# Kernel optimization log

Measured on AMD Instinct MI355X. Metric: run time of the kernel, lower is better.

Reference implementation:

```python
import jax, jax.numpy as jnp
import numpy as np

NEG_INF = -1e8  # masked_fill value from the torch code
EPS_DICE = 0.001
EPS_DIV = 1e-5
LOSS_FACTOR = 1.0  # loss['factor']


def conv2d(x, w, b, pad):
    # x: [B,C,H,W], w: [O,I,kh,kw] (OIHW), b: [O]
    y = jax.lax.conv_general_dilated(
        x, w, window_strides=(1, 1), padding=[(pad, pad), (pad, pad)],
        dimension_numbers=("NCHW", "OIHW", "NCHW"))
    return y + b[None, :, None, None]


def setup_inputs() -> dict:
    key = jax.random.key(0)
    ks = jax.random.split(key, 12)
    B, C, H, W = 2, 256, 64, 64
    s = 0.05  # small init scale to keep logits in a sane range
    inp = {
        "feats": jax.random.normal(ks[0], (B, C, H, W), jnp.float32),
        "masks": jax.random.randint(ks[1], (B, H, W), 0, 2).astype(jnp.float32),
        "layouts": jax.random.randint(ks[2], (B, H, W), 0, 16).astype(jnp.int32),
        "w_pre0": jax.random.normal(ks[3], (C, C, 3, 3), jnp.float32) * s,
        "b_pre0": jax.random.normal(ks[4], (C,), jnp.float32) * s,
        "w_pre1": jax.random.normal(ks[5], (C, C, 3, 3), jnp.float32) * s,
        "b_pre1": jax.random.normal(ks[6], (C,), jnp.float32) * s,
        "w_kernel": jax.random.normal(ks[7], (C + 1, C, 1, 1), jnp.float32) * s,
        "b_kernel": jax.random.normal(ks[8], (C + 1,), jnp.float32) * s,
        "w_feats": jax.random.normal(ks[9], (C, C, 1, 1), jnp.float32) * s,
        "b_feats": jax.random.normal(ks[10], (C,), jnp.float32) * s,
    }
    return inp


def reference(feats, masks, layouts, w_pre0, b_pre0, w_pre1, b_pre1,
              w_kernel, b_kernel, w_feats, b_feats):
    B, C, H, W = feats.shape
    # pre_kernel_convs: two 3x3 conv + ReLU
    h = jax.nn.relu(conv2d(feats, w_pre0, b_pre0, pad=1))
    h = jax.nn.relu(conv2d(h, w_pre1, b_pre1, pad=1))
    kernels = conv2d(h, w_kernel, b_kernel, pad=0)          # [B, C+1, H, W]
    f = conv2d(feats, w_feats, b_feats, pad=0)               # [B, C,   H, W]
    # permute(0,2,3,1).reshape(B, H*W, C+1): per-cell dynamic 1x1 conv params
    kernels = kernels.transpose(0, 2, 3, 1).reshape(B, H * W, C + 1)
    kw = kernels[..., :C]                                    # [B, P, C]
    kb = kernels[..., C]                                     # [B, P]
    # grouped 1x1 conv == batched matmul over channel dim
    logits = jnp.einsum("bpc,bchw->bphw", kw, f) + kb[:, :, None, None]
    logits = jnp.where(masks[:, None, :, :] > 0, logits, NEG_INF)  # [B,P,H,W]

    # --- training loss (dice, div='all') ---
    # segm_labels[b, r*W+c] = (layouts[b] == layouts[b,r,c])
    flat = layouts.reshape(B, H * W)
    labels = (layouts[:, None, :, :] == flat[:, :, None, None]).astype(logits.dtype)
    p = jax.nn.sigmoid(logits)
    d = 2.0 * (p * labels) / (p * p + EPS_DICE + labels * labels + EPS_DICE)
    loss_el = 1.0 - d                                        # [B, P, H, W]
    m_flat = masks.reshape(B, H * W)
    num = ((loss_el * masks[:, None, :, :]).sum((-1, -2)) * m_flat).sum(-1)  # [B]
    grid = masks.sum((1, 2))
    loss = (LOSS_FACTOR * num / (grid * grid + EPS_DIV)).mean()
    return logits, loss
```

## Files before the change

### kernel.cpp

```cpp
#include <hip/hip_runtime.h>
#include <hip/hip_bf16.h>
#include <math.h>

typedef __attribute__((ext_vector_type(8))) short bf16x8;
typedef __attribute__((ext_vector_type(4))) float f32x4;
typedef __hip_bfloat16 bf16_t;

#define NEG_INF_V -100000000.0f

__device__ __forceinline__ void gload16(const void* g, void* l) {
  __builtin_amdgcn_global_load_lds(
      (const __attribute__((address_space(1))) unsigned int*)g,
      (__attribute__((address_space(3))) unsigned int*)l, 16, 0, 0);
}

__global__ __launch_bounds__(256) void pad_cast_k(
    const float* __restrict__ feats, bf16_t* __restrict__ x_pad) {
  __shared__ float s[64][65];
  const int t = threadIdx.x;
  const int y = blockIdx.x, c0 = blockIdx.y * 64, b = blockIdx.z;
  const float* fb = feats + ((size_t)b * 256 + c0) * 4096 + y * 64;
  for (int i = t; i < 64 * 64; i += 256) {
    int ci = i >> 6, x = i & 63;
    s[ci][x] = fb[(size_t)ci * 4096 + x];
  }
  __syncthreads();
  bf16_t* xp = x_pad + (size_t)b * (66 * 66 * 256) + ((size_t)(y + 1) * 66 + 1) * 256 + c0;
  for (int i = t; i < 64 * 64; i += 256) {
    int x = i >> 6, ci = i & 63;
    xp[(size_t)x * 256 + ci] = __float2bfloat16(s[ci][x]);
  }
}

__global__ __launch_bounds__(256) void castw3_k(
    const float* __restrict__ w0, const float* __restrict__ w1,
    bf16_t* __restrict__ o0, bf16_t* __restrict__ o1) {
  const int co = blockIdx.x, t = threadIdx.x;
  const float* ws = blockIdx.y ? w1 : w0;
  bf16_t* wd = blockIdx.y ? o1 : o0;
#pragma unroll
  for (int k = 0; k < 9; ++k)
    wd[(size_t)co * 2304 + k * 256 + t] = __float2bfloat16(ws[((size_t)co * 256 + t) * 9 + k]);
}

__global__ __launch_bounds__(256) void castw1_k(
    const float* __restrict__ wk, const float* __restrict__ wf,
    bf16_t* __restrict__ ok, bf16_t* __restrict__ of) {
  int i = blockIdx.x * 256 + threadIdx.x;
  if (i < 257 * 256) ok[i] = __float2bfloat16(wk[i]);
  else { int j = i - 257 * 256; if (j < 256 * 256) of[j] = __float2bfloat16(wf[j]); }
}

__global__ __launch_bounds__(256) void conv3x3_mfma_k(
    const bf16_t* __restrict__ xpad, const bf16_t* __restrict__ wr,
    const float* __restrict__ bias, bf16_t* __restrict__ out,
    int out_row_stride, int out_base, long out_bstride) {
  __shared__ __align__(16) short ldsA[64 * 32];
  __shared__ __align__(16) short ldsB[128 * 32];
  const int t = threadIdx.x, w = t >> 6, lane = t & 63;
  const int y = blockIdx.x, co0 = blockIdx.y * 128, b = blockIdx.z;
  const bf16_t* xb = xpad + (size_t)b * (66 * 66 * 256);
  const int wm = w >> 1, wn = w & 1;
  f32x4 acc[2][4] = {};
  const int spix = w * 16 + (lane >> 2);
  const int scio = (lane & 3) * 8;
  const int sbco = w * 32 + (lane >> 2);
  const int aoff = (wm * 32 + (lane & 15)) * 32 + (lane >> 4) * 8;
  const int boff = (wn * 64 + (lane & 15)) * 32 + (lane >> 4) * 8;
  short* ldsAw = &ldsA[w * 512];
  short* ldsBw0 = &ldsB[(w * 32) * 32];
  short* ldsBw1 = &ldsB[(w * 32 + 16) * 32];

  for (int ks = 0; ks < 72; ++ks) {
    const int kpos = ks >> 3, cik = (ks & 7) * 32;
    const int ky = (kpos * 11) >> 5, kx = kpos - 3 * ky;
    gload16(xb + ((size_t)(y + ky) * 66 + spix + kx) * 256 + cik + scio, ldsAw);
    const bf16_t* gb = wr + (size_t)(co0 + sbco) * 2304 + kpos * 256 + cik + scio;
    gload16(gb, ldsBw0);
    gload16(gb + 16 * 2304, ldsBw1);
    __syncthreads();
    bf16x8 af0 = *(const bf16x8*)&ldsA[aoff];
    bf16x8 af1 = *(const bf16x8*)&ldsA[aoff + 512];
#pragma unroll
    for (int n = 0; n < 4; ++n) {
      bf16x8 bf = *(const bf16x8*)&ldsB[boff + n * 512];
      acc[0][n] = __builtin_amdgcn_mfma_f32_16x16x32_bf16(af0, bf, acc[0][n], 0, 0, 0);
      acc[1][n] = __builtin_amdgcn_mfma_f32_16x16x32_bf16(af1, bf, acc[1][n], 0, 0, 0);
    }
    __syncthreads();
  }
  bf16_t* ob = out + (size_t)b * out_bstride;
  float bv[4];
#pragma unroll
  for (int n = 0; n < 4; ++n) bv[n] = bias[co0 + wn * 64 + n * 16 + (lane & 15)];
#pragma unroll
  for (int m = 0; m < 2; ++m) {
#pragma unroll
    for (int r = 0; r < 4; ++r) {
      int x = wm * 32 + m * 16 + (lane >> 4) * 4 + r;
      size_t ra = (size_t)out_base + (size_t)y * out_row_stride + (size_t)x * 256 + co0 + wn * 64 + (lane & 15);
#pragma unroll
      for (int n = 0; n < 4; ++n) {
        float v = acc[m][n][r] + bv[n];
        ob[ra + n * 16] = __float2bfloat16(fmaxf(v, 0.f));
      }
    }
  }
}

template <bool KER>
__global__ __launch_bounds__(256) void conv1x1_mfma_k(
    const bf16_t* __restrict__ in, const bf16_t* __restrict__ wt,
    const float* __restrict__ bias, bf16_t* __restrict__ outw,
    float* __restrict__ outkb, int A0, int AS, long in_bstride, int comax) {
  __shared__ __align__(16) short ldsA[64 * 32];
  __shared__ __align__(16) short ldsB[128 * 32];
  const int t = threadIdx.x, w = t >> 6, lane = t & 63;
  const int y = blockIdx.x, co0 = blockIdx.y * 128, b = blockIdx.z;
  const bf16_t* inb = in + (size_t)b * in_bstride;
  const int wm = w >> 1, wn = w & 1;
  f32x4 acc[2][4] = {};
  const int spix = w * 16 + (lane >> 2);
  const int scio = (lane & 3) * 8;
  const int sbco = co0 + w * 32 + (lane >> 2);
  const int aoff = (wm * 32 + (lane & 15)) * 32 + (lane >> 4) * 8;
  const int boff = (wn * 64 + (lane & 15)) * 32 + (lane >> 4) * 8;
  short* ldsAw = &ldsA[w * 512];
  short* ldsBw0 = &ldsB[(w * 32) * 32];
  short* ldsBw1 = &ldsB[(w * 32 + 16) * 32];

  for (int ks = 0; ks < 8; ++ks) {
    const int cik = ks * 32;
    gload16(inb + (size_t)A0 + (size_t)y * AS + (size_t)spix * 256 + cik + scio, ldsAw);
    int c0r = min(sbco, comax - 1), c1r = min(sbco + 16, comax - 1);
    gload16(wt + (size_t)c0r * 256 + cik + scio, ldsBw0);
    gload16(wt + (size_t)c1r * 256 + cik + scio, ldsBw1);
    __syncthreads();
    bf16x8 af0 = *(const bf16x8*)&ldsA[aoff];
    bf16x8 af1 = *(const bf16x8*)&ldsA[aoff + 512];
#pragma unroll
    for (int n = 0; n < 4; ++n) {
      bf16x8 bf = *(const bf16x8*)&ldsB[boff + n * 512];
      acc[0][n] = __builtin_amdgcn_mfma_f32_16x16x32_bf16(af0, bf, acc[0][n], 0, 0, 0);
      acc[1][n] = __builtin_amdgcn_mfma_f32_16x16x32_bf16(af1, bf, acc[1][n], 0, 0, 0);
    }
    __syncthreads();
  }
#pragma unroll
  for (int m = 0; m < 2; ++m) {
#pragma unroll
    for (int r = 0; r < 4; ++r) {
      int x = wm * 32 + m * 16 + (lane >> 4) * 4 + r;
      int prow = y * 64 + x;
#pragma unroll
      for (int n = 0; n < 4; ++n) {
        int co = co0 + wn * 64 + n * 16 + (lane & 15);
        float v = acc[m][n][r] + bias[min(co, comax - 1)];
        if (KER) {
          if (co < 256) outw[((size_t)b * 4096 + prow) * 256 + co] = __float2bfloat16(v);
          else if (co == 256) outkb[(size_t)b * 4096 + prow] = v;
        } else {
          outw[((size_t)b * 4096 + prow) * 256 + co] = __float2bfloat16(v);
        }
      }
    }
  }
}

__global__ __launch_bounds__(256) void logits_mfma_k(
    const bf16_t* __restrict__ kwt, const float* __restrict__ kb,
    const bf16_t* __restrict__ fft, const float* __restrict__ masks,
    const int* __restrict__ layouts, float* __restrict__ out,
    float* __restrict__ partial) {
  __shared__ __align__(16) short ldsA[64 * 32];
  __shared__ __align__(16) short ldsB[128 * 32];
  const int t = threadIdx.x, w = t >> 6, lane = t & 63;
  const int p0 = blockIdx.x * 64, q0 = blockIdx.y * 128, b = blockIdx.z;
  const bf16_t* ab = kwt + (size_t)b * (4096 * 256);
  const bf16_t* bb = fft + (size_t)b * (4096 * 256);
  const int wm = w >> 1, wn = w & 1;
  f32x4 acc[2][4] = {};
  const int spix = w * 16 + (lane >> 2);
  const int scio = (lane & 3) * 8;
  const int sbq = w * 32 + (lane >> 2);
  const int aoff = (wm * 32 + (lane & 15)) * 32 + (lane >> 4) * 8;
  const int boff = (wn * 64 + (lane & 15)) * 32 + (lane >> 4) * 8;
  short* ldsAw = &ldsA[w * 512];
  short* ldsBw0 = &ldsB[(w * 32) * 32];
  short* ldsBw1 = &ldsB[(w * 32 + 16) * 32];

  for (int ks = 0; ks < 8; ++ks) {
    const int cik = ks * 32;
    gload16(ab + (size_t)(p0 + spix) * 256 + cik + scio, ldsAw);
    gload16(bb + (size_t)(q0 + sbq) * 256 + cik + scio, ldsBw0);
    gload16(bb + (size_t)(q0 + sbq + 16) * 256 + cik + scio, ldsBw1);
    __syncthreads();
    bf16x8 af0 = *(const bf16x8*)&ldsA[aoff];
    bf16x8 af1 = *(const bf16x8*)&ldsA[aoff + 512];
#pragma unroll
    for (int n = 0; n < 4; ++n) {
      bf16x8 bf = *(const bf16x8*)&ldsB[boff + n * 512];
      acc[0][n] = __builtin_amdgcn_mfma_f32_16x16x32_bf16(af0, bf, acc[0][n], 0, 0, 0);
      acc[1][n] = __builtin_amdgcn_mfma_f32_16x16x32_bf16(af1, bf, acc[1][n], 0, 0, 0);
    }
    __syncthreads();
  }

  float mq[4];
  int layq[4];
#pragma unroll
  for (int n = 0; n < 4; ++n) {
    int q = q0 + wn * 64 + n * 16 + (lane & 15);
    mq[n] = masks[b * 4096 + q];
    layq[n] = layouts[b * 4096 + q];
  }
  float sl[8];
#pragma unroll
  for (int i = 0; i < 8; ++i) sl[i] = 0.f;
  float* outb = out + (size_t)b * 4096 * 4096;
#pragma unroll
  for (int m = 0; m < 2; ++m) {
#pragma unroll
    for (int r = 0; r < 4; ++r) {
      int p = p0 + wm * 32 + m * 16 + (lane >> 4) * 4 + r;
      float kbv = kb[b * 4096 + p];
      int layp = layouts[b * 4096 + p];
      float s = 0.f;
      size_t ra = (size_t)p * 4096 + q0 + wn * 64 + (lane & 15);
#pragma unroll
      for (int n = 0; n < 4; ++n) {
        float lg = (mq[n] > 0.f) ? (acc[m][n][r] + kbv) : NEG_INF_V;
        outb[ra + n * 16] = lg;
        float pz = 1.f / (1.f + __expf(-lg));
        float lab = (layp == layq[n]) ? 1.f : 0.f;
        float d = 2.f * pz * lab / (pz * pz + lab + 0.002f);
        s += (1.f - d) * mq[n];
      }
      sl[m * 4 + r] = s;
    }
  }
#pragma unroll
  for (int i = 0; i < 8; ++i) {
    float v = sl[i];
    v += __shfl_xor(v, 1); v += __shfl_xor(v, 2);
    v += __shfl_xor(v, 4); v += __shfl_xor(v, 8);
    sl[i] = v;
  }
  if ((lane & 15) == 0) {
    int qt = blockIdx.y * 2 + wn;
#pragma unroll
    for (int m = 0; m < 2; ++m)
#pragma unroll
      for (int r = 0; r < 4; ++r) {
        int p = p0 + wm * 32 + m * 16 + (lane >> 4) * 4 + r;
        partial[((size_t)b * 4096 + p) * 64 + qt] = sl[m * 4 + r];
      }
  }
}

__global__ __launch_bounds__(256) void rowsum_k(
    const float* __restrict__ partial, const float* __restrict__ masks,
    float* __restrict__ accum) {
  const int t = threadIdx.x, w = t >> 6, lane = t & 63;
  const int idx = blockIdx.x * 256 + t;
  const int b = idx >> 12;
  const float* pp = partial + (size_t)idx * 64;
  float s = 0.f;
#pragma unroll
  for (int k = 0; k < 64; ++k) s += pp[k];
  float mp = masks[idx];
  float num = s * mp;
#pragma unroll
  for (int off = 32; off; off >>= 1) {
    num += __shfl_down(num, off);
    mp += __shfl_down(mp, off);
  }
  __shared__ float sn[4], sm[4];
  if (lane == 0) { sn[w] = num; sm[w] = mp; }
  __syncthreads();
  if (t == 0) {
    atomicAdd(&accum[b * 2], sn[0] + sn[1] + sn[2] + sn[3]);
    atomicAdd(&accum[b * 2 + 1], sm[0] + sm[1] + sm[2] + sm[3]);
  }
}

__global__ void loss_final_k(const float* __restrict__ accum, float* __restrict__ out_loss) {
  if (threadIdx.x == 0) {
    float l0 = accum[0] / (accum[1] * accum[1] + 1e-5f);
    float l1 = accum[2] / (accum[3] * accum[3] + 1e-5f);
    out_loss[0] = 0.5f * (l0 + l1);
  }
}

extern "C" void kernel_launch(void* const* d_in, const int* in_sizes, int n_in,
                              void* d_out, int out_size, void* d_ws, size_t ws_size,
                              hipStream_t stream) {
  const float* feats = (const float*)d_in[0];
  const float* masks = (const float*)d_in[1];
  const int* layouts = (const int*)d_in[2];
  const float* w_pre0 = (const float*)d_in[3];
  const float* b_pre0 = (const float*)d_in[4];
  const float* w_pre1 = (const float*)d_in[5];
  const float* b_pre1 = (const float*)d_in[6];
  const float* w_kernel = (const float*)d_in[7];
  const float* b_kernel = (const float*)d_in[8];
  const float* w_feats = (const float*)d_in[9];
  const float* b_feats = (const float*)d_in[10];

  bf16_t* x_pad = (bf16_t*)d_ws;
  bf16_t* h1p = x_pad + 2 * 1115136;
  bf16_t* h2 = h1p + 2 * 1115136;
  bf16_t* w0r = h2 + 2 * 1048576;
  bf16_t* w1r = w0r + 589824;
  bf16_t* wkb = w1r + 589824;
  bf16_t* wfb = wkb + 65792;
  bf16_t* kwt = wfb + 65536;
  bf16_t* fft = kwt + 2 * 1048576;
  float* kb = (float*)(fft + 2 * 1048576);
  float* partial = kb + 8192;
  float* accum = partial + 524288;
  float* out = (float*)d_out;

  hipMemsetAsync(x_pad, 0, (size_t)4 * 1115136 * sizeof(bf16_t), stream);
  hipMemsetAsync(accum, 0, 4 * sizeof(float), stream);

  pad_cast_k<<<dim3(64, 4, 2), 256, 0, stream>>>(feats, x_pad);
  castw3_k<<<dim3(256, 2), 256, 0, stream>>>(w_pre0, w_pre1, w0r, w1r);
  castw1_k<<<dim3(514), 256, 0, stream>>>(w_kernel, w_feats, wkb, wfb);

  conv3x3_mfma_k<<<dim3(64, 2, 2), 256, 0, stream>>>(
      x_pad, w0r, b_pre0, h1p, 66 * 256, 67 * 256, 1115136L);
  conv3x3_mfma_k<<<dim3(64, 2, 2), 256, 0, stream>>>(
      h1p, w1r, b_pre1, h2, 64 * 256, 0, 1048576L);

  conv1x1_mfma_k<true><<<dim3(64, 3, 2), 256, 0, stream>>>(
      h2, wkb, b_kernel, kwt, kb, 0, 16384, 1048576L, 257);
  conv1x1_mfma_k<false><<<dim3(64, 2, 2), 256, 0, stream>>>(
      x_pad, wfb, b_feats, fft, nullptr, 67 * 256, 66 * 256, 1115136L, 256);

  logits_mfma_k<<<dim3(64, 32, 2), 256, 0, stream>>>(
      kwt, kb, fft, masks, layouts, out, partial);

  rowsum_k<<<dim3(32), 256, 0, stream>>>(partial, masks, accum);
  loss_final_k<<<1, 64, 0, stream>>>(accum, out + (size_t)2 * 4096 * 4096);
}
```

Measured before the change: 304.0 us.

## Double-buffer LDS with XOR swizzle and K=64 stages in MFMA GEMM kernels

Rewrites the conv3x3, conv1x1 and logits MFMA kernels so that they load K-slices of 64 into double-buffered LDS. The next slice is prefetched while the current one is computed, which halves the barriers per K step. LDS reads use an XOR swizzle to avoid bank conflicts. The conv kernels also shrink the output-channel tile from 128 to 64 and double the grid, giving more blocks for occupancy in exchange for more re-reads of the activations.

```diff
diff --git a/kernel.cpp b/kernel.cpp
--- a/kernel.cpp
+++ b/kernel.cpp
@@ -12,6 +12,10 @@
   __builtin_amdgcn_global_load_lds(
       (const __attribute__((address_space(1))) unsigned int*)g,
       (__attribute__((address_space(3))) unsigned int*)l, 16, 0, 0);
+}
+
+__device__ __forceinline__ bf16x8 swzread(const short* base, int r, int c) {
+  return *(const bf16x8*)(base + ((r * 8 + (c ^ (r & 7))) << 3));
 }
 
 __global__ __launch_bounds__(256) void pad_cast_k(
@@ -55,57 +59,75 @@
     const bf16_t* __restrict__ xpad, const bf16_t* __restrict__ wr,
     const float* __restrict__ bias, bf16_t* __restrict__ out,
     int out_row_stride, int out_base, long out_bstride) {
-  __shared__ __align__(16) short ldsA[64 * 32];
-  __shared__ __align__(16) short ldsB[128 * 32];
+  __shared__ __align__(16) short ldsA[2][4096];
+  __shared__ __align__(16) short ldsB[2][4096];
   const int t = threadIdx.x, w = t >> 6, lane = t & 63;
-  const int y = blockIdx.x, co0 = blockIdx.y * 128, b = blockIdx.z;
+  const int y = blockIdx.x, co0 = blockIdx.y * 64, b = blockIdx.z;
   const bf16_t* xb = xpad + (size_t)b * (66 * 66 * 256);
   const int wm = w >> 1, wn = w & 1;
-  f32x4 acc[2][4] = {};
-  const int spix = w * 16 + (lane >> 2);
-  const int scio = (lane & 3) * 8;
-  const int sbco = w * 32 + (lane >> 2);
-  const int aoff = (wm * 32 + (lane & 15)) * 32 + (lane >> 4) * 8;
-  const int boff = (wn * 64 + (lane & 15)) * 32 + (lane >> 4) * 8;
-  short* ldsAw = &ldsA[w * 512];
-  short* ldsBw0 = &ldsB[(w * 32) * 32];
-  short* ldsBw1 = &ldsB[(w * 32 + 16) * 32];
-
-  for (int ks = 0; ks < 72; ++ks) {
-    const int kpos = ks >> 3, cik = (ks & 7) * 32;
-    const int ky = (kpos * 11) >> 5, kx = kpos - 3 * ky;
-    gload16(xb + ((size_t)(y + ky) * 66 + spix + kx) * 256 + cik + scio, ldsAw);
-    const bf16_t* gb = wr + (size_t)(co0 + sbco) * 2304 + kpos * 256 + cik + scio;
-    gload16(gb, ldsBw0);
-    gload16(gb + 16 * 2304, ldsBw1);
+  f32x4 acc[2][2] = {};
+
+  int ar[2], ac[2];
+#pragma unroll
+  for (int p = 0; p < 2; ++p) {
+    int u = (p * 4 + w) * 64 + lane;
+    ar[p] = u >> 3;
+    ac[p] = ((u & 7) ^ ((u >> 3) & 7)) * 8;
+  }
+  const int fr = lane & 15, fc = lane >> 4;
+
+  auto stage = [&](int ks, int buf) {
+    int kpos = ks >> 2, cik = (ks & 3) * 64;
+    int ky = (kpos * 11) >> 5, kx = kpos - 3 * ky;
+#pragma unroll
+    for (int p = 0; p < 2; ++p) {
+      gload16(xb + ((size_t)(y + ky) * 66 + (ar[p] + kx)) * 256 + cik + ac[p],
+              &ldsA[buf][(p * 4 + w) * 512]);
+      gload16(wr + (size_t)(co0 + ar[p]) * 2304 + kpos * 256 + cik + ac[p],
+              &ldsB[buf][(p * 4 + w) * 512]);
+    }
+  };
+  auto compute = [&](int buf) {
+#pragma unroll
+    for (int kk = 0; kk < 2; ++kk) {
+      bf16x8 af[2], bfr[2];
+#pragma unroll
+      for (int m = 0; m < 2; ++m) af[m] = swzread(ldsA[buf], wm * 32 + m * 16 + fr, kk * 4 + fc);
+#pragma unroll
+      for (int n = 0; n < 2; ++n) bfr[n] = swzread(ldsB[buf], wn * 32 + n * 16 + fr, kk * 4 + fc);
+#pragma unroll
+      for (int m = 0; m < 2; ++m)
+#pragma unroll
+        for (int n = 0; n < 2; ++n)
+          acc[m][n] = __builtin_amdgcn_mfma_f32_16x16x32_bf16(af[m], bfr[n], acc[m][n], 0, 0, 0);
+    }
+  };
+
+  stage(0, 0);
+  __syncthreads();
+  for (int ks = 0; ks < 35; ++ks) {
+    stage(ks + 1, (ks + 1) & 1);
+    compute(ks & 1);
     __syncthreads();
-    bf16x8 af0 = *(const bf16x8*)&ldsA[aoff];
-    bf16x8 af1 = *(const bf16x8*)&ldsA[aoff + 512];
-#pragma unroll
-    for (int n = 0; n < 4; ++n) {
-      bf16x8 bf = *(const bf16x8*)&ldsB[boff + n * 512];
-      acc[0][n] = __builtin_amdgcn_mfma_f32_16x16x32_bf16(af0, bf, acc[0][n], 0, 0, 0);
-      acc[1][n] = __builtin_amdgcn_mfma_f32_16x16x32_bf16(af1, bf, acc[1][n], 0, 0, 0);
-    }
-    __syncthreads();
-  }
+  }
+  compute(1);
+
   bf16_t* ob = out + (size_t)b * out_bstride;
-  float bv[4];
-#pragma unroll
-  for (int n = 0; n < 4; ++n) bv[n] = bias[co0 + wn * 64 + n * 16 + (lane & 15)];
-#pragma unroll
-  for (int m = 0; m < 2; ++m) {
+  float bv[2];
+#pragma unroll
+  for (int n = 0; n < 2; ++n) bv[n] = bias[co0 + wn * 32 + n * 16 + fr];
+#pragma unroll
+  for (int m = 0; m < 2; ++m)
 #pragma unroll
     for (int r = 0; r < 4; ++r) {
-      int x = wm * 32 + m * 16 + (lane >> 4) * 4 + r;
-      size_t ra = (size_t)out_base + (size_t)y * out_row_stride + (size_t)x * 256 + co0 + wn * 64 + (lane & 15);
-#pragma unroll
-      for (int n = 0; n < 4; ++n) {
+      int x = wm * 32 + m * 16 + fc * 4 + r;
+      size_t ra = (size_t)out_base + (size_t)y * out_row_stride + (size_t)x * 256 + co0 + wn * 32 + fr;
+#pragma unroll
+      for (int n = 0; n < 2; ++n) {
         float v = acc[m][n][r] + bv[n];
         ob[ra + n * 16] = __float2bfloat16(fmaxf(v, 0.f));
       }
     }
-  }
 }
 
 template <bool KER>
@@ -113,48 +135,67 @@
     const bf16_t* __restrict__ in, const bf16_t* __restrict__ wt,
     const float* __restrict__ bias, bf16_t* __restrict__ outw,
     float* __restrict__ outkb, int A0, int AS, long in_bstride, int comax) {
-  __shared__ __align__(16) short ldsA[64 * 32];
-  __shared__ __align__(16) short ldsB[128 * 32];
+  __shared__ __align__(16) short ldsA[2][4096];
+  __shared__ __align__(16) short ldsB[2][4096];
   const int t = threadIdx.x, w = t >> 6, lane = t & 63;
-  const int y = blockIdx.x, co0 = blockIdx.y * 128, b = blockIdx.z;
+  const int y = blockIdx.x, co0 = blockIdx.y * 64, b = blockIdx.z;
   const bf16_t* inb = in + (size_t)b * in_bstride;
   const int wm = w >> 1, wn = w & 1;
-  f32x4 acc[2][4] = {};
-  const int spix = w * 16 + (lane >> 2);
-  const int scio = (lane & 3) * 8;
-  const int sbco = co0 + w * 32 + (lane >> 2);
-  const int aoff = (wm * 32 + (lane & 15)) * 32 + (lane >> 4) * 8;
-  const int boff = (wn * 64 + (lane & 15)) * 32 + (lane >> 4) * 8;
-  short* ldsAw = &ldsA[w * 512];
-  short* ldsBw0 = &ldsB[(w * 32) * 32];
-  short* ldsBw1 = &ldsB[(w * 32 + 16) * 32];
-
-  for (int ks = 0; ks < 8; ++ks) {
-    const int cik = ks * 32;
-    gload16(inb + (size_t)A0 + (size_t)y * AS + (size_t)spix * 256 + cik + scio, ldsAw);
-    int c0r = min(sbco, comax - 1), c1r = min(sbco + 16, comax - 1);
-    gload16(wt + (size_t)c0r * 256 + cik + scio, ldsBw0);
-    gload16(wt + (size_t)c1r * 256 + cik + scio, ldsBw1);
+  f32x4 acc[2][2] = {};
+
+  int ar[2], ac[2];
+#pragma unroll
+  for (int p = 0; p < 2; ++p) {
+    int u = (p * 4 + w) * 64 + lane;
+    ar[p] = u >> 3;
+    ac[p] = ((u & 7) ^ ((u >> 3) & 7)) * 8;
+  }
+  const int fr = lane & 15, fc = lane >> 4;
+
+  auto stage = [&](int ks, int buf) {
+    int cik = ks * 64;
+#pragma unroll
+    for (int p = 0; p < 2; ++p) {
+      gload16(inb + (size_t)A0 + (size_t)y * AS + (size_t)ar[p] * 256 + cik + ac[p],
+              &ldsA[buf][(p * 4 + w) * 512]);
+      gload16(wt + (size_t)min(co0 + ar[p], comax - 1) * 256 + cik + ac[p],
+              &ldsB[buf][(p * 4 + w) * 512]);
+    }
+  };
+  auto compute = [&](int buf) {
+#pragma unroll
+    for (int kk = 0; kk < 2; ++kk) {
+      bf16x8 af[2], bfr[2];
+#pragma unroll
+      for (int m = 0; m < 2; ++m) af[m] = swzread(ldsA[buf], wm * 32 + m * 16 + fr, kk * 4 + fc);
+#pragma unroll
+      for (int n = 0; n < 2; ++n) bfr[n] = swzread(ldsB[buf], wn * 32 + n * 16 + fr, kk * 4 + fc);
+#pragma unroll
+      for (int m = 0; m < 2; ++m)
+#pragma unroll
+        for (int n = 0; n < 2; ++n)
+          acc[m][n] = __builtin_amdgcn_mfma_f32_16x16x32_bf16(af[m], bfr[n], acc[m][n], 0, 0, 0);
+    }
+  };
+
+  stage(0, 0);
+  __syncthreads();
+  for (int ks = 0; ks < 3; ++ks) {
+    stage(ks + 1, (ks + 1) & 1);
+    compute(ks & 1);
     __syncthreads();
-    bf16x8 af0 = *(const bf16x8*)&ldsA[aoff];
-    bf16x8 af1 = *(const bf16x8*)&ldsA[aoff + 512];
-#pragma unroll
-    for (int n = 0; n < 4; ++n) {
-      bf16x8 bf = *(const bf16x8*)&ldsB[boff + n * 512];
-      acc[0][n] = __builtin_amdgcn_mfma_f32_16x16x32_bf16(af0, bf, acc[0][n], 0, 0, 0);
-      acc[1][n] = __builtin_amdgcn_mfma_f32_16x16x32_bf16(af1, bf, acc[1][n], 0, 0, 0);
-    }
-    __syncthreads();
-  }
-#pragma unroll
-  for (int m = 0; m < 2; ++m) {
+  }
+  compute(1);
+
+#pragma unroll
+  for (int m = 0; m < 2; ++m)
 #pragma unroll
     for (int r = 0; r < 4; ++r) {
-      int x = wm * 32 + m * 16 + (lane >> 4) * 4 + r;
+      int x = wm * 32 + m * 16 + fc * 4 + r;
       int prow = y * 64 + x;
 #pragma unroll
-      for (int n = 0; n < 4; ++n) {
-        int co = co0 + wn * 64 + n * 16 + (lane & 15);
+      for (int n = 0; n < 2; ++n) {
+        int co = co0 + wn * 32 + n * 16 + fr;
         float v = acc[m][n][r] + bias[min(co, comax - 1)];
         if (KER) {
           if (co < 256) outw[((size_t)b * 4096 + prow) * 256 + co] = __float2bfloat16(v);
@@ -164,7 +205,6 @@
         }
       }
     }
-  }
 }
 
 __global__ __launch_bounds__(256) void logits_mfma_k(
@@ -172,45 +212,69 @@
     const bf16_t* __restrict__ fft, const float* __restrict__ masks,
     const int* __restrict__ layouts, float* __restrict__ out,
     float* __restrict__ partial) {
-  __shared__ __align__(16) short ldsA[64 * 32];
-  __shared__ __align__(16) short ldsB[128 * 32];
+  __shared__ __align__(16) short ldsA[2][4096];
+  __shared__ __align__(16) short ldsB[2][8192];
   const int t = threadIdx.x, w = t >> 6, lane = t & 63;
   const int p0 = blockIdx.x * 64, q0 = blockIdx.y * 128, b = blockIdx.z;
   const bf16_t* ab = kwt + (size_t)b * (4096 * 256);
   const bf16_t* bb = fft + (size_t)b * (4096 * 256);
   const int wm = w >> 1, wn = w & 1;
   f32x4 acc[2][4] = {};
-  const int spix = w * 16 + (lane >> 2);
-  const int scio = (lane & 3) * 8;
-  const int sbq = w * 32 + (lane >> 2);
-  const int aoff = (wm * 32 + (lane & 15)) * 32 + (lane >> 4) * 8;
-  const int boff = (wn * 64 + (lane & 15)) * 32 + (lane >> 4) * 8;
-  short* ldsAw = &ldsA[w * 512];
-  short* ldsBw0 = &ldsB[(w * 32) * 32];
-  short* ldsBw1 = &ldsB[(w * 32 + 16) * 32];
-
-  for (int ks = 0; ks < 8; ++ks) {
-    const int cik = ks * 32;
-    gload16(ab + (size_t)(p0 + spix) * 256 + cik + scio, ldsAw);
-    gload16(bb + (size_t)(q0 + sbq) * 256 + cik + scio, ldsBw0);
-    gload16(bb + (size_t)(q0 + sbq + 16) * 256 + cik + scio, ldsBw1);
+
+  int ar[2], ac[2], br[4], bc[4];
+#pragma unroll
+  for (int p = 0; p < 2; ++p) {
+    int u = (p * 4 + w) * 64 + lane;
+    ar[p] = u >> 3;
+    ac[p] = ((u & 7) ^ ((u >> 3) & 7)) * 8;
+  }
+#pragma unroll
+  for (int p = 0; p < 4; ++p) {
+    int u = (p * 4 + w) * 64 + lane;
+    br[p] = u >> 3;
+    bc[p] = ((u & 7) ^ ((u >> 3) & 7)) * 8;
+  }
+  const int fr = lane & 15, fc = lane >> 4;
+
+  auto stage = [&](int ks, int buf) {
+    int cik = ks * 64;
+#pragma unroll
+    for (int p = 0; p < 2; ++p)
+      gload16(ab + (size_t)(p0 + ar[p]) * 256 + cik + ac[p], &ldsA[buf][(p * 4 + w) * 512]);
+#pragma unroll
+    for (int p = 0; p < 4; ++p)
+      gload16(bb + (size_t)(q0 + br[p]) * 256 + cik + bc[p], &ldsB[buf][(p * 4 + w) * 512]);
+  };
+  auto compute = [&](int buf) {
+#pragma unroll
+    for (int kk = 0; kk < 2; ++kk) {
+      bf16x8 af[2], bfr[4];
+#pragma unroll
+      for (int m = 0; m < 2; ++m) af[m] = swzread(ldsA[buf], wm * 32 + m * 16 + fr, kk * 4 + fc);
+#pragma unroll
+      for (int n = 0; n < 4; ++n) bfr[n] = swzread(ldsB[buf], wn * 64 + n * 16 + fr, kk * 4 + fc);
+#pragma unroll
+      for (int m = 0; m < 2; ++m)
+#pragma unroll
+        for (int n = 0; n < 4; ++n)
+          acc[m][n] = __builtin_amdgcn_mfma_f32_16x16x32_bf16(af[m], bfr[n], acc[m][n], 0, 0, 0);
+    }
+  };
+
+  stage(0, 0);
+  __syncthreads();
+  for (int ks = 0; ks < 3; ++ks) {
+    stage(ks + 1, (ks + 1) & 1);
+    compute(ks & 1);
     __syncthreads();
-    bf16x8 af0 = *(const bf16x8*)&ldsA[aoff];
-    bf16x8 af1 = *(const bf16x8*)&ldsA[aoff + 512];
-#pragma unroll
-    for (int n = 0; n < 4; ++n) {
-      bf16x8 bf = *(const bf16x8*)&ldsB[boff + n * 512];
-      acc[0][n] = __builtin_amdgcn_mfma_f32_16x16x32_bf16(af0, bf, acc[0][n], 0, 0, 0);
-      acc[1][n] = __builtin_amdgcn_mfma_f32_16x16x32_bf16(af1, bf, acc[1][n], 0, 0, 0);
-    }
-    __syncthreads();
-  }
+  }
+  compute(1);
 
   float mq[4];
   int layq[4];
 #pragma unroll
   for (int n = 0; n < 4; ++n) {
-    int q = q0 + wn * 64 + n * 16 + (lane & 15);
+    int q = q0 + wn * 64 + n * 16 + fr;
     mq[n] = masks[b * 4096 + q];
     layq[n] = layouts[b * 4096 + q];
   }
@@ -222,11 +286,11 @@
   for (int m = 0; m < 2; ++m) {
 #pragma unroll
     for (int r = 0; r < 4; ++r) {
-      int p = p0 + wm * 32 + m * 16 + (lane >> 4) * 4 + r;
+      int p = p0 + wm * 32 + m * 16 + fc * 4 + r;
       float kbv = kb[b * 4096 + p];
       int layp = layouts[b * 4096 + p];
       float s = 0.f;
-      size_t ra = (size_t)p * 4096 + q0 + wn * 64 + (lane & 15);
+      size_t ra = (size_t)p * 4096 + q0 + wn * 64 + fr;
 #pragma unroll
       for (int n = 0; n < 4; ++n) {
         float lg = (mq[n] > 0.f) ? (acc[m][n][r] + kbv) : NEG_INF_V;
@@ -246,13 +310,13 @@
     v += __shfl_xor(v, 4); v += __shfl_xor(v, 8);
     sl[i] = v;
   }
-  if ((lane & 15) == 0) {
+  if (fr == 0) {
     int qt = blockIdx.y * 2 + wn;
 #pragma unroll
     for (int m = 0; m < 2; ++m)
 #pragma unroll
       for (int r = 0; r < 4; ++r) {
-        int p = p0 + wm * 32 + m * 16 + (lane >> 4) * 4 + r;
+        int p = p0 + wm * 32 + m * 16 + fc * 4 + r;
         partial[((size_t)b * 4096 + p) * 64 + qt] = sl[m * 4 + r];
       }
   }
@@ -328,14 +392,14 @@
   castw3_k<<<dim3(256, 2), 256, 0, stream>>>(w_pre0, w_pre1, w0r, w1r);
   castw1_k<<<dim3(514), 256, 0, stream>>>(w_kernel, w_feats, wkb, wfb);
 
-  conv3x3_mfma_k<<<dim3(64, 2, 2), 256, 0, stream>>>(
+  conv3x3_mfma_k<<<dim3(64, 4, 2), 256, 0, stream>>>(
       x_pad, w0r, b_pre0, h1p, 66 * 256, 67 * 256, 1115136L);
-  conv3x3_mfma_k<<<dim3(64, 2, 2), 256, 0, stream>>>(
+  conv3x3_mfma_k<<<dim3(64, 4, 2), 256, 0, stream>>>(
       h1p, w1r, b_pre1, h2, 64 * 256, 0, 1048576L);
 
-  conv1x1_mfma_k<true><<<dim3(64, 3, 2), 256, 0, stream>>>(
+  conv1x1_mfma_k<true><<<dim3(64, 5, 2), 256, 0, stream>>>(
       h2, wkb, b_kernel, kwt, kb, 0, 16384, 1048576L, 257);
-  conv1x1_mfma_k<false><<<dim3(64, 2, 2), 256, 0, stream>>>(
+  conv1x1_mfma_k<false><<<dim3(64, 4, 2), 256, 0, stream>>>(
       x_pad, wfb, b_feats, fft, nullptr, 67 * 256, 66 * 256, 1115136L, 256);
 
   logits_mfma_k<<<dim3(64, 32, 2), 256, 0, stream>>>(
```

Measured after the change: 283.4 us. 6.8% less time.
